# Optimization experiments

Measured on AMD Instinct MI355X. Metric: run time of the kernel, lower is better.

Reference implementation:

```python
import jax, jax.numpy as jnp
import numpy as np

NUM_HEADS = 8
EMBED_DIM = 128
HEAD_DIM = EMBED_DIM // NUM_HEADS  # 16
NB_FEATURES = EMBED_DIM            # 128
EPS = 1e-4


def _make_projection(nb_rows, nb_cols, rng):
    # gaussian_orthogonal_random_matrix with scaling=0
    blocks = []
    for _ in range(nb_rows // nb_cols):
        q, _ = np.linalg.qr(rng.standard_normal((nb_cols, nb_cols)))
        blocks.append(q.T)
    rem = nb_rows - (nb_rows // nb_cols) * nb_cols
    if rem > 0:
        q, _ = np.linalg.qr(rng.standard_normal((nb_cols, nb_cols)))
        blocks.append(q.T[:rem])
    final = np.concatenate(blocks, axis=0)
    mult = np.linalg.norm(rng.standard_normal((nb_rows, nb_cols)), axis=1)
    return (mult[:, None] * final).astype(np.float32)


def setup_inputs() -> dict:
    key = jax.random.key(0)
    ks = jax.random.split(key, 7)
    R, C, E = 8, 2048, EMBED_DIM
    s = 1.0 / np.sqrt(E)
    x = jax.random.normal(ks[0], (R, C, E), dtype=jnp.float32)
    Wq = jax.random.uniform(ks[1], (E, E), jnp.float32, -s, s)
    bq = jax.random.uniform(ks[2], (E,), jnp.float32, -s, s)
    Wk = jax.random.uniform(ks[3], (E, E), jnp.float32, -s, s)
    bk = jax.random.uniform(ks[4], (E,), jnp.float32, -s, s)
    Wv = jax.random.uniform(ks[5], (E, E), jnp.float32, -s, s)
    bv = jax.random.uniform(ks[6], (E,), jnp.float32, -s, s)
    proj = jnp.asarray(_make_projection(NB_FEATURES, HEAD_DIM, np.random.default_rng(0)))
    return {"x": x, "Wq": Wq, "bq": bq, "Wk": Wk, "bk": bk, "Wv": Wv, "bv": bv, "proj": proj}


def _softmax_kernel(data, proj, is_query):
    # data: (R, h, n, d); proj: (F, d)
    d = data.shape[-1]
    normalizer = d ** (-0.25)
    ratio = proj.shape[0] ** (-0.5)
    data_dash = jnp.einsum('rhnd,jd->rhnj', normalizer * data, proj)  # (R,h,n,F)
    diag = jnp.sum(data * data, axis=-1, keepdims=True) * 0.5 * normalizer ** 2
    if is_query:
        m = jnp.max(data_dash, axis=-1, keepdims=True)
    else:
        m = jnp.max(data_dash, axis=(-1, -2), keepdims=True)
    return ratio * (jnp.exp(data_dash - diag - m) + EPS)


def reference(x, Wq, bq, Wk, bk, Wv, bv, proj):
    R, C, E = x.shape
    h, hd = NUM_HEADS, HEAD_DIM

    def proj_heads(W, b):
        y = jnp.einsum('rce,fe->rcf', x, W) + b
        return y.reshape(R, C, h, hd).transpose(0, 2, 1, 3)  # (R,h,C,hd)

    q = _softmax_kernel(proj_heads(Wq, bq), proj, is_query=True)   # (R,h,C,F)
    k = _softmax_kernel(proj_heads(Wk, bk), proj, is_query=False)  # (R,h,C,F)
    v = proj_heads(Wv, bv)                                          # (R,h,C,hd)

    # fold batch (R) into the feature dim: (h, C, R*F) / (h, C, R*hd)
    qf = q.transpose(1, 2, 0, 3).reshape(h, C, R * NB_FEATURES)
    kf = k.transpose(1, 2, 0, 3).reshape(h, C, R * NB_FEATURES)
    vf = v.transpose(1, 2, 0, 3).reshape(h, C, R * hd)

    k_sum = kf.sum(axis=-2)                                   # (h, D)
    D_inv = 1.0 / jnp.einsum('hnd,hd->hn', qf, k_sum)         # (h, C)
    context = jnp.einsum('hnd,hne->hde', kf, vf)              # (h, D, Ev)
    out = jnp.einsum('hde,hnd,hn->hne', context, qf, D_inv)   # (h, C, R*hd)

    out = out.reshape(h, C, R, hd).transpose(2, 1, 0, 3).reshape(R, C, E)
    attn = jnp.einsum('hqf,hkf->hqk', qf, kf)                 # (h, C, C)
    return out, attn
```

## Files before the change

kernel.cpp:

```cpp
#include <hip/hip_runtime.h>
#include <hip/hip_bf16.h>
#include <stdint.h>

typedef __bf16 bf16x8 __attribute__((ext_vector_type(8)));
typedef float  f32x4  __attribute__((ext_vector_type(4)));

#define RATIO 0.08838834764831845f
#define EPSV  1e-4f

#define GLOBAL_AS __attribute__((address_space(1)))
#define LDS_AS    __attribute__((address_space(3)))

static __device__ __forceinline__ void gload16(const void* g, void* l) {
  __builtin_amdgcn_global_load_lds((GLOBAL_AS const void*)g, (LDS_AS void*)l, 16, 0, 0);
}

static constexpr size_t OFF_XB    = 0;
static constexpr size_t OFF_WCAT  = OFF_XB    + 4194304;
static constexpr size_t OFF_MQ    = OFF_WCAT  + 98304;
static constexpr size_t OFF_MK    = OFF_MQ    + 262144;
static constexpr size_t OFF_BCAT  = OFF_MK    + 262144;
static constexpr size_t OFF_BQF   = OFF_BCAT  + 2048;
static constexpr size_t OFF_BKF   = OFF_BQF   + 4096;
static constexpr size_t OFF_Y     = OFF_BKF   + 4096;
static constexpr size_t OFF_QF    = OFF_Y     + 25165824;
static constexpr size_t OFF_KF    = OFF_QF    + 33554432;
static constexpr size_t OFF_KFT   = OFF_KF    + 33554432;
static constexpr size_t OFF_VFT   = OFF_KFT   + 33554432;
static constexpr size_t OFF_KPART = OFF_VFT   + 4194304;
static constexpr size_t OFF_KMAX  = OFF_KPART + 4096;
static constexpr size_t OFF_KSUM  = OFF_KMAX  + 256;
static constexpr size_t OFF_DINV  = OFF_KSUM  + 32768;
static constexpr size_t OFF_CTXP  = OFF_DINV  + 65536;
static constexpr size_t OFF_CTXT  = OFF_CTXP  + 16777216;
static constexpr size_t WS_NEED   = OFF_CTXT  + 2097152;

static __device__ __forceinline__ void gemm_core(
    const __hip_bfloat16* __restrict__ A, const __hip_bfloat16* __restrict__ B,
    int lda, int ldb, int K, int tm, int tn,
    __bf16* As, __bf16* Bs, f32x4 acc[4][4]) {
  const int t    = threadIdx.x;
  const int w    = t >> 6;
  const int lane = t & 63;
  const int m_off = (w >> 1) << 6;
  const int n_off = (w & 1) << 6;
  const int r0 = t >> 2;
  const int kk = (t & 3) << 3;
  char* Asb = (char*)As + (w << 10);
  char* Bsb = (char*)Bs + (w << 10);
  const int frow = lane & 15;
  const int koff = (lane >> 4) << 3;
  for (int k0 = 0; k0 < K; k0 += 32) {
    const __hip_bfloat16* Ag = A + (size_t)(tm + r0) * lda + (k0 + kk);
    const __hip_bfloat16* Bg = B + (size_t)(tn + r0) * ldb + (k0 + kk);
    gload16(Ag, Asb);
    gload16(Ag + (size_t)64 * lda, Asb + 4096);
    gload16(Bg, Bsb);
    gload16(Bg + (size_t)64 * ldb, Bsb + 4096);
    __syncthreads();
    bf16x8 af[4], bfr[4];
#pragma unroll
    for (int mi = 0; mi < 4; ++mi)
      af[mi] = *(const bf16x8*)(As + ((m_off + mi * 16 + frow) << 5) + koff);
#pragma unroll
    for (int ni = 0; ni < 4; ++ni)
      bfr[ni] = *(const bf16x8*)(Bs + ((n_off + ni * 16 + frow) << 5) + koff);
#pragma unroll
    for (int mi = 0; mi < 4; ++mi)
#pragma unroll
      for (int ni = 0; ni < 4; ++ni)
        acc[mi][ni] = __builtin_amdgcn_mfma_f32_16x16x32_bf16(af[mi], bfr[ni], acc[mi][ni], 0, 0, 0);
    __syncthreads();
  }
}

#define ZERO_ACC(acc) do {                                   \
  _Pragma("unroll") for (int a_ = 0; a_ < 4; ++a_)           \
  _Pragma("unroll") for (int b_ = 0; b_ < 4; ++b_)           \
    acc[a_][b_] = (f32x4){0.f, 0.f, 0.f, 0.f};               \
} while (0)

__global__ void k_prep(const float* __restrict__ x,
                       const float* __restrict__ Wq, const float* __restrict__ bq,
                       const float* __restrict__ Wk, const float* __restrict__ bk,
                       const float* __restrict__ Wv, const float* __restrict__ bv,
                       const float* __restrict__ proj,
                       __hip_bfloat16* __restrict__ xb,
                       __hip_bfloat16* __restrict__ Wcat, float* __restrict__ bcat,
                       __hip_bfloat16* __restrict__ Mq, __hip_bfloat16* __restrict__ Mk,
                       float* __restrict__ bqf, float* __restrict__ bkf) {
  const int b = blockIdx.x, t = threadIdx.x;
  {
    int i = (b * 256 + t) * 4;
    f32x4 v = *(const f32x4*)(x + i);
#pragma unroll
    for (int j = 0; j < 4; ++j) xb[i + j] = __float2bfloat16(v[j]);
  }
  if (b < 1024) {
    int i = b * 256 + t;
    {
      int which = i >> 17;
      int rem = i & 131071;
      int hj = rem >> 7, e = rem & 127;
      int hh = hj >> 7, j = hj & 127;
      const float* W = which ? Wk : Wq;
      float s = 0.f;
#pragma unroll
      for (int u = 0; u < 16; ++u) s += proj[j * 16 + u] * W[(hh * 16 + u) * 128 + e];
      if (which) Mk[rem] = __float2bfloat16(0.5f * s);
      else       Mq[rem] = __float2bfloat16(0.5f * s);
    }
    if (i < 2048) {
      int which = i >> 10;
      int hj = i & 1023, hh = hj >> 7, j = hj & 127;
      const float* bb = which ? bk : bq;
      float s = 0.f;
#pragma unroll
      for (int u = 0; u < 16; ++u) s += proj[j * 16 + u] * bb[hh * 16 + u];
      if (which) bkf[hj] = 0.5f * s;
      else       bqf[hj] = 0.5f * s;
    }
  }
  if (b < 192) {
    int i = b * 256 + t;
    int mat = i >> 14, rem = i & 16383;
    const float* W = (mat == 0) ? Wq : ((mat == 1) ? Wk : Wv);
    Wcat[i] = __float2bfloat16(W[rem]);
    if (i < 384) {
      int m2 = i >> 7;
      const float* bb = (m2 == 0) ? bq : ((m2 == 1) ? bk : bv);
      bcat[i] = bb[i & 127];
    }
  }
}

__global__ __launch_bounds__(256) void k_proj(
    const __hip_bfloat16* __restrict__ xb, const __hip_bfloat16* __restrict__ Wcat,
    const float* __restrict__ bcat, float* __restrict__ Y) {
  __shared__ __align__(16) __bf16 As[4096], Bs[4096];
  const int tm = blockIdx.x << 7, tn = blockIdx.y << 7;
  f32x4 acc[4][4];
  ZERO_ACC(acc);
  gemm_core(xb, Wcat, 128, 128, 128, tm, tn, As, Bs, acc);
  const int t = threadIdx.x, w = t >> 6, lane = t & 63;
  const int m_off = (w >> 1) << 6, n_off = (w & 1) << 6;
#pragma unroll
  for (int ni = 0; ni < 4; ++ni) {
    const int col = tn + n_off + ni * 16 + (lane & 15);
    const float bias = bcat[col];
#pragma unroll
    for (int mi = 0; mi < 4; ++mi)
#pragma unroll
      for (int i = 0; i < 4; ++i) {
        const int row = tm + m_off + mi * 16 + ((lane >> 4) << 2) + i;
        Y[(size_t)row * 384 + col] = acc[mi][ni][i] + bias;
      }
  }
}

__global__ void k_vft2(const float* __restrict__ Y, __hip_bfloat16* __restrict__ vfT) {
  const int cb = blockIdx.x, r = blockIdx.y, h = blockIdx.z;
  const int c0 = cb << 7;
  __shared__ float tile[16][132];
  const int t = threadIdx.x;
  const int a = t & 15, cc0 = t >> 4;
#pragma unroll
  for (int i = 0; i < 8; ++i) {
    const int cc = cc0 + (i << 4);
    tile[a][cc] = Y[(size_t)(r * 2048 + c0 + cc) * 384 + 256 + (h << 4) + a];
  }
  __syncthreads();
  const int row = t >> 4, cg = t & 15;
  bf16x8 v;
#pragma unroll
  for (int j = 0; j < 8; ++j) v[j] = (__bf16)tile[row][(cg << 3) + j];
  *(bf16x8*)(vfT + ((size_t)((h << 7) + (r << 4) + row) << 11) + c0 + (cg << 3)) = v;
}

__global__ __launch_bounds__(256) void k_dashq(
    const __hip_bfloat16* __restrict__ xb, const __hip_bfloat16* __restrict__ Mq,
    const float* __restrict__ bqf, const float* __restrict__ Y,
    __hip_bfloat16* __restrict__ qf) {
  __shared__ __align__(16) __bf16 As[4096], Bs[4096];
  __shared__ float diag_s[128];
  __shared__ float rmax_s[2][128];
  const int h = blockIdx.y;
  const int tm = blockIdx.x << 7;
  f32x4 acc[4][4];
  ZERO_ACC(acc);
  gemm_core(xb, Mq + h * 16384, 128, 128, 128, tm, 0, As, Bs, acc);
  const int t = threadIdx.x, w = t >> 6, lane = t & 63;
  const int m_off = (w >> 1) << 6, n_off = (w & 1) << 6;
  if (t < 128) {
    const float* yp = Y + (size_t)(tm + t) * 384 + h * 16;
    float s = 0.f;
#pragma unroll
    for (int u = 0; u < 16; ++u) s += yp[u] * yp[u];
    diag_s[t] = 0.125f * s;
  }
  float bia[4];
#pragma unroll
  for (int ni = 0; ni < 4; ++ni) bia[ni] = bqf[h * 128 + n_off + ni * 16 + (lane & 15)];
  float rmx[4][4];
#pragma unroll
  for (int mi = 0; mi < 4; ++mi)
#pragma unroll
    for (int i = 0; i < 4; ++i) {
      float m0 = acc[mi][0][i] + bia[0];
      m0 = fmaxf(m0, acc[mi][1][i] + bia[1]);
      m0 = fmaxf(m0, acc[mi][2][i] + bia[2]);
      m0 = fmaxf(m0, acc[mi][3][i] + bia[3]);
      rmx[mi][i] = m0;
    }
#pragma unroll
  for (int off = 1; off < 16; off <<= 1)
#pragma unroll
    for (int mi = 0; mi < 4; ++mi)
#pragma unroll
      for (int i = 0; i < 4; ++i)
        rmx[mi][i] = fmaxf(rmx[mi][i], __shfl_xor(rmx[mi][i], off));
  if ((lane & 15) == 0) {
#pragma unroll
    for (int mi = 0; mi < 4; ++mi)
#pragma unroll
      for (int i = 0; i < 4; ++i)
        rmax_s[w & 1][m_off + mi * 16 + ((lane >> 4) << 2) + i] = rmx[mi][i];
  }
  __syncthreads();
#pragma unroll
  for (int mi = 0; mi < 4; ++mi) {
#pragma unroll
    for (int i = 0; i < 4; ++i) {
      const int rl = m_off + mi * 16 + ((lane >> 4) << 2) + i;
      const int rg = tm + rl;
      const int c = rg & 2047, r = rg >> 11;
      const float md = diag_s[rl] + fmaxf(rmax_s[0][rl], rmax_s[1][rl]);
#pragma unroll
      for (int ni = 0; ni < 4; ++ni) {
        const int j = n_off + ni * 16 + (lane & 15);
        const float f = RATIO * (__expf(acc[mi][ni][i] + bia[ni] - md) + EPSV);
        qf[((size_t)((h << 11) + c) << 10) + (r << 7) + j] = __float2bfloat16(f);
      }
    }
  }
}

__global__ __launch_bounds__(256) void k_dashk_max(
    const __hip_bfloat16* __restrict__ xb, const __hip_bfloat16* __restrict__ Mk,
    const float* __restrict__ bkf, float* __restrict__ kpart) {
  __shared__ __align__(16) __bf16 As[4096], Bs[4096];
  __shared__ float wmax[4];
  const int h = blockIdx.y;
  const int tm = blockIdx.x << 7;
  f32x4 acc[4][4];
  ZERO_ACC(acc);
  gemm_core(xb, Mk + h * 16384, 128, 128, 128, tm, 0, As, Bs, acc);
  const int t = threadIdx.x, w = t >> 6, lane = t & 63;
  const int n_off = (w & 1) << 6;
  float mx = -1e30f;
#pragma unroll
  for (int ni = 0; ni < 4; ++ni) {
    const float bia = bkf[h * 128 + n_off + ni * 16 + (lane & 15)];
#pragma unroll
    for (int mi = 0; mi < 4; ++mi)
#pragma unroll
      for (int i = 0; i < 4; ++i) mx = fmaxf(mx, acc[mi][ni][i] + bia);
  }
#pragma unroll
  for (int off = 1; off < 64; off <<= 1) mx = fmaxf(mx, __shfl_xor(mx, off));
  if (lane == 0) wmax[w] = mx;
  __syncthreads();
  if (t == 0) kpart[h * 128 + blockIdx.x] = fmaxf(fmaxf(wmax[0], wmax[1]), fmaxf(wmax[2], wmax[3]));
}

__global__ void k_kmaxred(const float* __restrict__ kpart, float* __restrict__ kmax) {
  const int t = threadIdx.x;
  const int r = t >> 3, h = t & 7;
  float m = -1e30f;
  for (int i = 0; i < 16; ++i) m = fmaxf(m, kpart[h * 128 + r * 16 + i]);
  kmax[r * 8 + h] = m;
}

__global__ __launch_bounds__(256) void k_dashk_feat(
    const __hip_bfloat16* __restrict__ xb, const __hip_bfloat16* __restrict__ Mk,
    const float* __restrict__ bkf, const float* __restrict__ Y,
    const float* __restrict__ kmax,
    __hip_bfloat16* __restrict__ kf, __hip_bfloat16* __restrict__ kfT) {
  __shared__ __align__(16) __bf16 As[4096], Bs[4096];
  __shared__ float diag_s[128];
  __shared__ __align__(16) __bf16 kT[128 * 136];
  const int h = blockIdx.y;
  const int tm = blockIdx.x << 7;
  f32x4 acc[4][4];
  ZERO_ACC(acc);
  gemm_core(xb, Mk + h * 16384, 128, 128, 128, tm, 0, As, Bs, acc);
  const int t = threadIdx.x, w = t >> 6, lane = t & 63;
  const int m_off = (w >> 1) << 6, n_off = (w & 1) << 6;
  if (t < 128) {
    const float* yp = Y + (size_t)(tm + t) * 384 + 128 + h * 16;
    float s = 0.f;
#pragma unroll
    for (int u = 0; u < 16; ++u) s += yp[u] * yp[u];
    diag_s[t] = 0.125f * s;
  }
  const int r = tm >> 11;
  const int c0 = tm & 2047;
  const float m = kmax[r * 8 + h];
  float bia[4];
#pragma unroll
  for (int ni = 0; ni < 4; ++ni) bia[ni] = bkf[h * 128 + n_off + ni * 16 + (lane & 15)];
  __syncthreads();
#pragma unroll
  for (int mi = 0; mi < 4; ++mi) {
#pragma unroll
    for (int i = 0; i < 4; ++i) {
      const int rl = m_off + mi * 16 + ((lane >> 4) << 2) + i;
      const int c = c0 + rl;
      const float dm = diag_s[rl] + m;
#pragma unroll
      for (int ni = 0; ni < 4; ++ni) {
        const int j = n_off + ni * 16 + (lane & 15);
        const float f = RATIO * (__expf(acc[mi][ni][i] + bia[ni] - dm) + EPSV);
        kf[((size_t)((h << 11) + c) << 10) + (r << 7) + j] = __float2bfloat16(f);
        kT[j * 136 + rl] = (__bf16)f;
      }
    }
  }
  __syncthreads();
  const int j2 = t >> 1, half = t & 1;
  __bf16* dst = (__bf16*)kfT + (((size_t)(h << 10) + (r << 7) + j2) << 11) + c0 + (half << 6);
  const __bf16* srcr = kT + j2 * 136 + (half << 6);
#pragma unroll
  for (int q8 = 0; q8 < 8; ++q8)
    *(bf16x8*)(dst + (q8 << 3)) = *(const bf16x8*)(srcr + (q8 << 3));
}

__global__ __launch_bounds__(256) void k_ksum2(const __hip_bfloat16* __restrict__ kfT,
                                               float* __restrict__ ksum) {
  const int t = threadIdx.x, w = t >> 6, lane = t & 63;
  const int row = blockIdx.x * 4 + w;
  const __bf16* p = (const __bf16*)kfT + ((size_t)row << 11);
  float s = 0.f;
#pragma unroll
  for (int q = 0; q < 4; ++q) {
    bf16x8 v = *(const bf16x8*)(p + ((lane + (q << 6)) << 3));
#pragma unroll
    for (int j = 0; j < 8; ++j) s += (float)v[j];
  }
#pragma unroll
  for (int off = 1; off < 64; off <<= 1) s += __shfl_xor(s, off);
  if (lane == 0) ksum[row] = s;
}

__global__ __launch_bounds__(256) void k_dinv(
    const __hip_bfloat16* __restrict__ qf, const float* __restrict__ ksum,
    float* __restrict__ dinv) {
  const int t = threadIdx.x, w = t >> 6, lane = t & 63;
  const int h = blockIdx.y;
  const int c = blockIdx.x * 4 + w;
  const __bf16* qp = (const __bf16*)qf + ((size_t)((h << 11) + c) << 10);
  const float* ks = ksum + h * 1024;
  const int d0 = lane << 4;
  bf16x8 v0 = *(const bf16x8*)(qp + d0);
  bf16x8 v1 = *(const bf16x8*)(qp + d0 + 8);
  float s = 0.f;
#pragma unroll
  for (int j = 0; j < 8; ++j) s += (float)v0[j] * ks[d0 + j] + (float)v1[j] * ks[d0 + 8 + j];
#pragma unroll
  for (int off = 1; off < 64; off <<= 1) s += __shfl_xor(s, off);
  if (lane == 0) dinv[(h << 11) + c] = 1.0f / s;
}

#define SBAR() __builtin_amdgcn_s_barrier()
#define FEN()  do { asm volatile("" ::: "memory"); __builtin_amdgcn_sched_barrier(0); } while (0)
#define PRIO1() __builtin_amdgcn_s_setprio(1)
#define PRIO0() __builtin_amdgcn_s_setprio(0)
#define VMW4() do { asm volatile("s_waitcnt vmcnt(4)" ::: "memory"); } while (0)
#define VMW0() do { asm volatile("s_waitcnt vmcnt(0)" ::: "memory"); } while (0)

#define MFMA16(nlo) do {                                                      \
  _Pragma("unroll") for (int mi_ = 0; mi_ < 8; ++mi_)                         \
  _Pragma("unroll") for (int nj_ = 0; nj_ < 2; ++nj_)                         \
    acc[mi_][(nlo) + nj_] = __builtin_amdgcn_mfma_f32_16x16x32_bf16(          \
        aR[mi_], bR[nj_], acc[mi_][(nlo) + nj_], 0, 0, 0);                    \
} while (0)

__global__ __launch_bounds__(512, 2) void k_attn8(
    const __hip_bfloat16* __restrict__ qf, const __hip_bfloat16* __restrict__ kf,
    float* __restrict__ attn) {
  extern __shared__ __align__(128) char lds[];
  const int lid = blockIdx.x;
  const int swz = ((lid & 7) << 6) + (lid >> 3);
  const int h  = swz >> 6;
  const int tm = ((swz >> 3) & 7) << 8;
  const int tn = (swz & 7) << 8;
  const __hip_bfloat16* Ag = qf + ((size_t)h << 21);
  const __hip_bfloat16* Bg = kf + ((size_t)h << 21);

  const int t = threadIdx.x, wid = t >> 6, lane = t & 63;
  const int f = lane & 15;
  const int wr = wid >> 2, wc = wid & 3;
  const int swzg = (((lane >> 4) ^ ((f >> 1) & 3)) << 4);
  const int aoff = ((wr << 7) + f) * 64 + swzg;
  const int boff = 65536 + ((wc << 6) + f) * 64 + swzg;
  const int srow = t >> 2;
  const int scol = (((t & 3) ^ ((t >> 3) & 3)) << 3);
  const int sdst = wid << 10;

  f32x4 acc[8][4] = {};
  bf16x8 aR[8], bR[2];

  auto stageA = [&](int buf, int kh, int k0) {
    char* d = lds + buf * 32768 + kh * 16384 + sdst;
    const __hip_bfloat16* g = Ag + (size_t)(tm + srow) * 1024 + k0 + (kh << 5) + scol;
    gload16(g, d);
    gload16(g + 128 * 1024, d + 8192);
  };
  auto stageB = [&](int buf, int kh, int k0) {
    char* d = lds + 65536 + buf * 32768 + kh * 16384 + sdst;
    const __hip_bfloat16* g = Bg + (size_t)(tn + srow) * 1024 + k0 + (kh << 5) + scol;
    gload16(g, d);
    gload16(g + 128 * 1024, d + 8192);
  };

  stageA(0, 0, 0); stageB(0, 0, 0); stageA(0, 1, 0); stageB(0, 1, 0);
  VMW4();
  SBAR(); FEN();

  for (int kt = 0; kt < 15; ++kt) {
    const int buf = kt & 1, nbuf = buf ^ 1;
    const int bo = buf * 32768;
    const int nk0 = (kt + 1) << 6;
#pragma unroll
    for (int mi = 0; mi < 8; ++mi) aR[mi] = *(const bf16x8*)(lds + bo + aoff + mi * 1024);
    bR[0] = *(const bf16x8*)(lds + bo + boff);
    bR[1] = *(const bf16x8*)(lds + bo + boff + 1024);
    stageA(nbuf, 0, nk0);
    PRIO1(); MFMA16(0); PRIO0();
    SBAR(); FEN();
    bR[0] = *(const bf16x8*)(lds + bo + boff + 2048);
    bR[1] = *(const bf16x8*)(lds + bo + boff + 3072);
    stageB(nbuf, 0, nk0);
    PRIO1(); MFMA16(2); PRIO0();
    VMW4();
    SBAR(); FEN();
#pragma unroll
    for (int mi = 0; mi < 8; ++mi) aR[mi] = *(const bf16x8*)(lds + bo + 16384 + aoff + mi * 1024);
    bR[0] = *(const bf16x8*)(lds + bo + 16384 + boff);
    bR[1] = *(const bf16x8*)(lds + bo + 16384 + boff + 1024);
    stageA(nbuf, 1, nk0);
    PRIO1(); MFMA16(0); PRIO0();
    SBAR(); FEN();
    bR[0] = *(const bf16x8*)(lds + bo + 16384 + boff + 2048);
    bR[1] = *(const bf16x8*)(lds + bo + 16384 + boff + 3072);
    stageB(nbuf, 1, nk0);
    PRIO1(); MFMA16(2); PRIO0();
    VMW4();
    SBAR(); FEN();
  }
  {
    const int bo = 32768;
#pragma unroll
    for (int mi = 0; mi < 8; ++mi) aR[mi] = *(const bf16x8*)(lds + bo + aoff + mi * 1024);
    bR[0] = *(const bf16x8*)(lds + bo + boff);
    bR[1] = *(const bf16x8*)(lds + bo + boff + 1024);
    PRIO1(); MFMA16(0); PRIO0();
    bR[0] = *(const bf16x8*)(lds + bo + boff + 2048);
    bR[1] = *(const bf16x8*)(lds + bo + boff + 3072);
    PRIO1(); MFMA16(2); PRIO0();
    VMW0();
    SBAR(); FEN();
#pragma unroll
    for (int mi = 0; mi < 8; ++mi) aR[mi] = *(const bf16x8*)(lds + bo + 16384 + aoff + mi * 1024);
    bR[0] = *(const bf16x8*)(lds + bo + 16384 + boff);
    bR[1] = *(const bf16x8*)(lds + bo + 16384 + boff + 1024);
    PRIO1(); MFMA16(0); PRIO0();
    bR[0] = *(const bf16x8*)(lds + bo + 16384 + boff + 2048);
    bR[1] = *(const bf16x8*)(lds + bo + 16384 + boff + 3072);
    PRIO1(); MFMA16(2); PRIO0();
  }

  float* Cc = attn + ((size_t)h << 22);
  const int rbase = tm + (wr << 7) + ((lane >> 4) << 2);
  const int cbase = tn + (wc << 6) + f;
#pragma unroll
  for (int mi = 0; mi < 8; ++mi)
#pragma unroll
    for (int i = 0; i < 4; ++i) {
      float* rp = Cc + ((size_t)(rbase + mi * 16 + i) << 11) + cbase;
#pragma unroll
      for (int ni = 0; ni < 4; ++ni) rp[ni * 16] = acc[mi][ni][i];
    }
}

__global__ __launch_bounds__(256) void k_ctx(
    const __hip_bfloat16* __restrict__ vfT, const __hip_bfloat16* __restrict__ kfT,
    float* __restrict__ ctxp) {
  __shared__ __align__(16) __bf16 As[4096], Bs[4096];
  const int z = blockIdx.z, h = z >> 2, kc = z & 3;
  const int tn = blockIdx.y << 7;
  f32x4 acc[4][4];
  ZERO_ACC(acc);
  gemm_core(vfT + ((size_t)h << 18) + (kc << 9), kfT + ((size_t)h << 21) + (kc << 9),
            2048, 2048, 512, 0, tn, As, Bs, acc);
  float* Cp = ctxp + ((size_t)(kc * 8 + h) << 17);
  const int t = threadIdx.x, w = t >> 6, lane = t & 63;
  const int m_off = (w >> 1) << 6, n_off = (w & 1) << 6;
#pragma unroll
  for (int mi = 0; mi < 4; ++mi)
#pragma unroll
    for (int i = 0; i < 4; ++i) {
      const int row = m_off + mi * 16 + ((lane >> 4) << 2) + i;
#pragma unroll
      for (int ni = 0; ni < 4; ++ni) {
        const int col = tn + n_off + ni * 16 + (lane & 15);
        Cp[((size_t)row << 10) + col] = acc[mi][ni][i];
      }
    }
}

__global__ void k_ctxred(const float* __restrict__ ctxp, __hip_bfloat16* __restrict__ ctxT) {
  const int i = blockIdx.x * 256 + threadIdx.x;
  const float s = ctxp[i] + ctxp[i + 1048576] + ctxp[i + 2097152] + ctxp[i + 3145728];
  ctxT[i] = __float2bfloat16(s);
}

__global__ __launch_bounds__(256) void k_out(
    const __hip_bfloat16* __restrict__ qf, const __hip_bfloat16* __restrict__ ctxT,
    const float* __restrict__ dinv, float* __restrict__ outp) {
  __shared__ __align__(16) __bf16 As[4096], Bs[4096];
  const int h = blockIdx.z;
  const int tm = blockIdx.x << 7;
  f32x4 acc[4][4];
  ZERO_ACC(acc);
  gemm_core(qf + ((size_t)h << 21), ctxT + ((size_t)h << 17), 1024, 1024, 1024, tm, 0, As, Bs, acc);
  const int t = threadIdx.x, w = t >> 6, lane = t & 63;
  const int m_off = (w >> 1) << 6, n_off = (w & 1) << 6;
#pragma unroll
  for (int mi = 0; mi < 4; ++mi)
#pragma unroll
    for (int i = 0; i < 4; ++i) {
      const int row = tm + m_off + mi * 16 + ((lane >> 4) << 2) + i;
      const float dv = dinv[(h << 11) + row];
#pragma unroll
      for (int ni = 0; ni < 4; ++ni) {
        const int col = n_off + ni * 16 + (lane & 15);
        const int rb = col >> 4, tt = col & 15;
        outp[(((size_t)(rb << 11) + row) << 7) + (h << 4) + tt] = acc[mi][ni][i] * dv;
      }
    }
}

extern "C" void kernel_launch(void* const* d_in, const int* in_sizes, int n_in,
                              void* d_out, int out_size, void* d_ws, size_t ws_size,
                              hipStream_t stream) {
  const float* x    = (const float*)d_in[0];
  const float* Wq   = (const float*)d_in[1];
  const float* bq   = (const float*)d_in[2];
  const float* Wk   = (const float*)d_in[3];
  const float* bk   = (const float*)d_in[4];
  const float* Wv   = (const float*)d_in[5];
  const float* bv   = (const float*)d_in[6];
  const float* proj = (const float*)d_in[7];
  if (ws_size < WS_NEED) return;

  char* ws = (char*)d_ws;
  __hip_bfloat16* xb   = (__hip_bfloat16*)(ws + OFF_XB);
  __hip_bfloat16* Wcat = (__hip_bfloat16*)(ws + OFF_WCAT);
  __hip_bfloat16* Mq   = (__hip_bfloat16*)(ws + OFF_MQ);
  __hip_bfloat16* Mk   = (__hip_bfloat16*)(ws + OFF_MK);
  float* bcat = (float*)(ws + OFF_BCAT);
  float* bqf  = (float*)(ws + OFF_BQF);
  float* bkf  = (float*)(ws + OFF_BKF);
  float* Y    = (float*)(ws + OFF_Y);
  __hip_bfloat16* qf  = (__hip_bfloat16*)(ws + OFF_QF);
  __hip_bfloat16* kf  = (__hip_bfloat16*)(ws + OFF_KF);
  __hip_bfloat16* kfT = (__hip_bfloat16*)(ws + OFF_KFT);
  __hip_bfloat16* vfT = (__hip_bfloat16*)(ws + OFF_VFT);
  float* kpart = (float*)(ws + OFF_KPART);
  float* kmax  = (float*)(ws + OFF_KMAX);
  float* ksum  = (float*)(ws + OFF_KSUM);
  float* dinv  = (float*)(ws + OFF_DINV);
  float* ctxp  = (float*)(ws + OFF_CTXP);
  __hip_bfloat16* ctxT = (__hip_bfloat16*)(ws + OFF_CTXT);

  float* outp = (float*)d_out;
  float* attn = (float*)d_out + 2097152;

  static int attr_done = 0;
  if (!attr_done) {
    (void)hipFuncSetAttribute((const void*)k_attn8,
                              hipFuncAttributeMaxDynamicSharedMemorySize, 131072);
    attr_done = 1;
  }

  k_prep<<<dim3(2048), dim3(256), 0, stream>>>(x, Wq, bq, Wk, bk, Wv, bv, proj,
                                               xb, Wcat, bcat, Mq, Mk, bqf, bkf);
  k_proj<<<dim3(128, 3), dim3(256), 0, stream>>>(xb, Wcat, bcat, Y);
  k_vft2<<<dim3(16, 8, 8), dim3(256), 0, stream>>>(Y, vfT);
  k_dashq<<<dim3(128, 8), dim3(256), 0, stream>>>(xb, Mq, bqf, Y, qf);
  k_dashk_max<<<dim3(128, 8), dim3(256), 0, stream>>>(xb, Mk, bkf, kpart);
  k_kmaxred<<<dim3(1), dim3(64), 0, stream>>>(kpart, kmax);
  k_dashk_feat<<<dim3(128, 8), dim3(256), 0, stream>>>(xb, Mk, bkf, Y, kmax, kf, kfT);
  k_ksum2<<<dim3(2048), dim3(256), 0, stream>>>(kfT, ksum);
  k_dinv<<<dim3(512, 8), dim3(256), 0, stream>>>(qf, ksum, dinv);
  k_attn8<<<dim3(512), dim3(512), 131072, stream>>>(qf, kf, attn);
  k_ctx<<<dim3(1, 8, 32), dim3(256), 0, stream>>>(vfT, kfT, ctxp);
  k_ctxred<<<dim3(4096), dim3(256), 0, stream>>>(ctxp, ctxT);
  k_out<<<dim3(16, 1, 8), dim3(256), 0, stream>>>(qf, ctxT, dinv, outp);
}
```

Baseline: 201.5 us.

## Fuse Q/K feature GEMMs, atomic key max, fold ksum and dinv into ctx/out

Merges the query and key feature GEMMs into one kernel that shares the x tile. The per-(r,h) key max is now taken with an atomicMax on an order-preserving unsigned key, and the key logits are stored as fp16. A separate elementwise kernel then applies exp and writes kf/kfT. This removes the second key GEMM and the max-reduction launch. The key column sums move into the ctx GEMM's B-fragment loads, and the D_inv dot product moves into the out GEMM's main loop, which drops the ksum and dinv kernels. In exchange it adds a 32MB fp16 intermediate write and read, with some precision risk from storing the logits in fp16.

```diff
diff --git a/kernel.cpp b/kernel.cpp
--- a/kernel.cpp
+++ b/kernel.cpp
@@ -3,6 +3,7 @@
 #include <stdint.h>
 
 typedef __bf16 bf16x8 __attribute__((ext_vector_type(8)));
+typedef _Float16 f16x8 __attribute__((ext_vector_type(8)));
 typedef float  f32x4  __attribute__((ext_vector_type(4)));
 
 #define RATIO 0.08838834764831845f
@@ -13,6 +14,15 @@
 
 static __device__ __forceinline__ void gload16(const void* g, void* l) {
   __builtin_amdgcn_global_load_lds((GLOBAL_AS const void*)g, (LDS_AS void*)l, 16, 0, 0);
+}
+
+static __device__ __forceinline__ unsigned fkey(float f) {
+  unsigned b = __float_as_uint(f);
+  return (b & 0x80000000u) ? ~b : (b | 0x80000000u);
+}
+static __device__ __forceinline__ float funkey(unsigned k) {
+  unsigned b = (k & 0x80000000u) ? (k & 0x7FFFFFFFu) : ~k;
+  return __uint_as_float(b);
 }
 
 static constexpr size_t OFF_XB    = 0;
@@ -27,11 +37,10 @@
 static constexpr size_t OFF_KF    = OFF_QF    + 33554432;
 static constexpr size_t OFF_KFT   = OFF_KF    + 33554432;
 static constexpr size_t OFF_VFT   = OFF_KFT   + 33554432;
-static constexpr size_t OFF_KPART = OFF_VFT   + 4194304;
-static constexpr size_t OFF_KMAX  = OFF_KPART + 4096;
-static constexpr size_t OFF_KSUM  = OFF_KMAX  + 256;
-static constexpr size_t OFF_DINV  = OFF_KSUM  + 32768;
-static constexpr size_t OFF_CTXP  = OFF_DINV  + 65536;
+static constexpr size_t OFF_KMAXI = OFF_VFT   + 4194304;
+static constexpr size_t OFF_KSUMP = OFF_KMAXI + 1024;
+static constexpr size_t OFF_EK    = OFF_KSUMP + 131072;
+static constexpr size_t OFF_CTXP  = OFF_EK    + 33554432;
 static constexpr size_t OFF_CTXT  = OFF_CTXP  + 16777216;
 static constexpr size_t WS_NEED   = OFF_CTXT  + 2097152;
 
@@ -88,7 +97,8 @@
                        __hip_bfloat16* __restrict__ xb,
                        __hip_bfloat16* __restrict__ Wcat, float* __restrict__ bcat,
                        __hip_bfloat16* __restrict__ Mq, __hip_bfloat16* __restrict__ Mk,
-                       float* __restrict__ bqf, float* __restrict__ bkf) {
+                       float* __restrict__ bqf, float* __restrict__ bkf,
+                       unsigned* __restrict__ kmaxI) {
   const int b = blockIdx.x, t = threadIdx.x;
   {
     int i = (b * 256 + t) * 4;
@@ -96,6 +106,7 @@
 #pragma unroll
     for (int j = 0; j < 4; ++j) xb[i + j] = __float2bfloat16(v[j]);
   }
+  if (b == 0 && t < 64) kmaxI[t] = 0u;
   if (b < 1024) {
     int i = b * 256 + t;
     {
@@ -177,39 +188,84 @@
   *(bf16x8*)(vfT + ((size_t)((h << 7) + (r << 4) + row) << 11) + c0 + (cg << 3)) = v;
 }
 
-__global__ __launch_bounds__(256) void k_dashq(
+__global__ __launch_bounds__(256) void k_dashqk(
     const __hip_bfloat16* __restrict__ xb, const __hip_bfloat16* __restrict__ Mq,
-    const float* __restrict__ bqf, const float* __restrict__ Y,
-    __hip_bfloat16* __restrict__ qf) {
-  __shared__ __align__(16) __bf16 As[4096], Bs[4096];
-  __shared__ float diag_s[128];
+    const __hip_bfloat16* __restrict__ Mk, const float* __restrict__ bqf,
+    const float* __restrict__ bkf, const float* __restrict__ Y,
+    __hip_bfloat16* __restrict__ qf, _Float16* __restrict__ ek,
+    unsigned* __restrict__ kmaxI) {
+  __shared__ __align__(16) __bf16 As[4096], Bqs[4096], Bks[4096];
+  __shared__ float diagq_s[128], diagk_s[128];
   __shared__ float rmax_s[2][128];
+  __shared__ float wmax_s[4];
   const int h = blockIdx.y;
   const int tm = blockIdx.x << 7;
-  f32x4 acc[4][4];
-  ZERO_ACC(acc);
-  gemm_core(xb, Mq + h * 16384, 128, 128, 128, tm, 0, As, Bs, acc);
   const int t = threadIdx.x, w = t >> 6, lane = t & 63;
   const int m_off = (w >> 1) << 6, n_off = (w & 1) << 6;
+  const int r0 = t >> 2, kk = (t & 3) << 3;
+  char* Asb = (char*)As + (w << 10);
+  char* Bqb = (char*)Bqs + (w << 10);
+  char* Bkb = (char*)Bks + (w << 10);
+  const int frow = lane & 15, koff = (lane >> 4) << 3;
+  const __hip_bfloat16* Bq_ = Mq + h * 16384;
+  const __hip_bfloat16* Bk_ = Mk + h * 16384;
   if (t < 128) {
     const float* yp = Y + (size_t)(tm + t) * 384 + h * 16;
     float s = 0.f;
 #pragma unroll
     for (int u = 0; u < 16; ++u) s += yp[u] * yp[u];
-    diag_s[t] = 0.125f * s;
-  }
-  float bia[4];
-#pragma unroll
-  for (int ni = 0; ni < 4; ++ni) bia[ni] = bqf[h * 128 + n_off + ni * 16 + (lane & 15)];
+    diagq_s[t] = 0.125f * s;
+  } else {
+    const int tt = t - 128;
+    const float* yp = Y + (size_t)(tm + tt) * 384 + 128 + h * 16;
+    float s = 0.f;
+#pragma unroll
+    for (int u = 0; u < 16; ++u) s += yp[u] * yp[u];
+    diagk_s[tt] = 0.125f * s;
+  }
+  f32x4 accq[4][4], acck[4][4];
+  ZERO_ACC(accq); ZERO_ACC(acck);
+  for (int k0 = 0; k0 < 128; k0 += 32) {
+    const __hip_bfloat16* Ag = xb + (size_t)(tm + r0) * 128 + (k0 + kk);
+    const __hip_bfloat16* Bg1 = Bq_ + (size_t)r0 * 128 + (k0 + kk);
+    const __hip_bfloat16* Bg2 = Bk_ + (size_t)r0 * 128 + (k0 + kk);
+    gload16(Ag, Asb);  gload16(Ag + 64 * 128, Asb + 4096);
+    gload16(Bg1, Bqb); gload16(Bg1 + 64 * 128, Bqb + 4096);
+    gload16(Bg2, Bkb); gload16(Bg2 + 64 * 128, Bkb + 4096);
+    __syncthreads();
+    bf16x8 af[4], bq1[4], bk1[4];
+#pragma unroll
+    for (int mi = 0; mi < 4; ++mi)
+      af[mi] = *(const bf16x8*)(As + ((m_off + mi * 16 + frow) << 5) + koff);
+#pragma unroll
+    for (int ni = 0; ni < 4; ++ni) {
+      bq1[ni] = *(const bf16x8*)(Bqs + ((n_off + ni * 16 + frow) << 5) + koff);
+      bk1[ni] = *(const bf16x8*)(Bks + ((n_off + ni * 16 + frow) << 5) + koff);
+    }
+#pragma unroll
+    for (int mi = 0; mi < 4; ++mi)
+#pragma unroll
+      for (int ni = 0; ni < 4; ++ni) {
+        accq[mi][ni] = __builtin_amdgcn_mfma_f32_16x16x32_bf16(af[mi], bq1[ni], accq[mi][ni], 0, 0, 0);
+        acck[mi][ni] = __builtin_amdgcn_mfma_f32_16x16x32_bf16(af[mi], bk1[ni], acck[mi][ni], 0, 0, 0);
+      }
+    __syncthreads();
+  }
+  float biaq[4], biak[4];
+#pragma unroll
+  for (int ni = 0; ni < 4; ++ni) {
+    biaq[ni] = bqf[h * 128 + n_off + ni * 16 + frow];
+    biak[ni] = bkf[h * 128 + n_off + ni * 16 + frow];
+  }
   float rmx[4][4];
 #pragma unroll
   for (int mi = 0; mi < 4; ++mi)
 #pragma unroll
     for (int i = 0; i < 4; ++i) {
-      float m0 = acc[mi][0][i] + bia[0];
-      m0 = fmaxf(m0, acc[mi][1][i] + bia[1]);
-      m0 = fmaxf(m0, acc[mi][2][i] + bia[2]);
-      m0 = fmaxf(m0, acc[mi][3][i] + bia[3]);
+      float m0 = accq[mi][0][i] + biaq[0];
+      m0 = fmaxf(m0, accq[mi][1][i] + biaq[1]);
+      m0 = fmaxf(m0, accq[mi][2][i] + biaq[2]);
+      m0 = fmaxf(m0, accq[mi][3][i] + biaq[3]);
       rmx[mi][i] = m0;
     }
 #pragma unroll
@@ -219,112 +275,72 @@
 #pragma unroll
       for (int i = 0; i < 4; ++i)
         rmx[mi][i] = fmaxf(rmx[mi][i], __shfl_xor(rmx[mi][i], off));
-  if ((lane & 15) == 0) {
+  if (frow == 0) {
 #pragma unroll
     for (int mi = 0; mi < 4; ++mi)
 #pragma unroll
       for (int i = 0; i < 4; ++i)
         rmax_s[w & 1][m_off + mi * 16 + ((lane >> 4) << 2) + i] = rmx[mi][i];
   }
+  float mxk = -1e30f;
+#pragma unroll
+  for (int ni = 0; ni < 4; ++ni)
+#pragma unroll
+    for (int mi = 0; mi < 4; ++mi)
+#pragma unroll
+      for (int i = 0; i < 4; ++i) mxk = fmaxf(mxk, acck[mi][ni][i] + biak[ni]);
+#pragma unroll
+  for (int off = 1; off < 64; off <<= 1) mxk = fmaxf(mxk, __shfl_xor(mxk, off));
+  if (lane == 0) wmax_s[w] = mxk;
   __syncthreads();
+  const int r = tm >> 11;
+  if (t == 0) {
+    float bm = fmaxf(fmaxf(wmax_s[0], wmax_s[1]), fmaxf(wmax_s[2], wmax_s[3]));
+    atomicMax(&kmaxI[r * 8 + h], fkey(bm));
+  }
 #pragma unroll
   for (int mi = 0; mi < 4; ++mi) {
 #pragma unroll
     for (int i = 0; i < 4; ++i) {
       const int rl = m_off + mi * 16 + ((lane >> 4) << 2) + i;
       const int rg = tm + rl;
-      const int c = rg & 2047, r = rg >> 11;
-      const float md = diag_s[rl] + fmaxf(rmax_s[0][rl], rmax_s[1][rl]);
+      const int c = rg & 2047;
+      const float mdq = diagq_s[rl] + fmaxf(rmax_s[0][rl], rmax_s[1][rl]);
+      const float dk = diagk_s[rl];
 #pragma unroll
       for (int ni = 0; ni < 4; ++ni) {
-        const int j = n_off + ni * 16 + (lane & 15);
-        const float f = RATIO * (__expf(acc[mi][ni][i] + bia[ni] - md) + EPSV);
-        qf[((size_t)((h << 11) + c) << 10) + (r << 7) + j] = __float2bfloat16(f);
+        const int j = n_off + ni * 16 + frow;
+        const float fq = RATIO * (__expf(accq[mi][ni][i] + biaq[ni] - mdq) + EPSV);
+        qf[((size_t)((h << 11) + c) << 10) + (r << 7) + j] = __float2bfloat16(fq);
+        ek[((size_t)h << 21) + ((size_t)rg << 7) + j] = (_Float16)(acck[mi][ni][i] + biak[ni] - dk);
       }
     }
   }
 }
 
-__global__ __launch_bounds__(256) void k_dashk_max(
-    const __hip_bfloat16* __restrict__ xb, const __hip_bfloat16* __restrict__ Mk,
-    const float* __restrict__ bkf, float* __restrict__ kpart) {
-  __shared__ __align__(16) __bf16 As[4096], Bs[4096];
-  __shared__ float wmax[4];
-  const int h = blockIdx.y;
-  const int tm = blockIdx.x << 7;
-  f32x4 acc[4][4];
-  ZERO_ACC(acc);
-  gemm_core(xb, Mk + h * 16384, 128, 128, 128, tm, 0, As, Bs, acc);
-  const int t = threadIdx.x, w = t >> 6, lane = t & 63;
-  const int n_off = (w & 1) << 6;
-  float mx = -1e30f;
-#pragma unroll
-  for (int ni = 0; ni < 4; ++ni) {
-    const float bia = bkf[h * 128 + n_off + ni * 16 + (lane & 15)];
-#pragma unroll
-    for (int mi = 0; mi < 4; ++mi)
-#pragma unroll
-      for (int i = 0; i < 4; ++i) mx = fmaxf(mx, acc[mi][ni][i] + bia);
-  }
-#pragma unroll
-  for (int off = 1; off < 64; off <<= 1) mx = fmaxf(mx, __shfl_xor(mx, off));
-  if (lane == 0) wmax[w] = mx;
-  __syncthreads();
-  if (t == 0) kpart[h * 128 + blockIdx.x] = fmaxf(fmaxf(wmax[0], wmax[1]), fmaxf(wmax[2], wmax[3]));
-}
-
-__global__ void k_kmaxred(const float* __restrict__ kpart, float* __restrict__ kmax) {
+__global__ __launch_bounds__(256) void k_kfeat(
+    const _Float16* __restrict__ ek, const unsigned* __restrict__ kmaxI,
+    __hip_bfloat16* __restrict__ kf, __hip_bfloat16* __restrict__ kfT) {
+  __shared__ __align__(16) __bf16 kT[128 * 136];
+  const int h = blockIdx.y, tm = blockIdx.x << 7;
+  const int r = tm >> 11, c0 = tm & 2047;
+  const float m = funkey(kmaxI[r * 8 + h]);
   const int t = threadIdx.x;
-  const int r = t >> 3, h = t & 7;
-  float m = -1e30f;
-  for (int i = 0; i < 16; ++i) m = fmaxf(m, kpart[h * 128 + r * 16 + i]);
-  kmax[r * 8 + h] = m;
-}
-
-__global__ __launch_bounds__(256) void k_dashk_feat(
-    const __hip_bfloat16* __restrict__ xb, const __hip_bfloat16* __restrict__ Mk,
-    const float* __restrict__ bkf, const float* __restrict__ Y,
-    const float* __restrict__ kmax,
-    __hip_bfloat16* __restrict__ kf, __hip_bfloat16* __restrict__ kfT) {
-  __shared__ __align__(16) __bf16 As[4096], Bs[4096];
-  __shared__ float diag_s[128];
-  __shared__ __align__(16) __bf16 kT[128 * 136];
-  const int h = blockIdx.y;
-  const int tm = blockIdx.x << 7;
-  f32x4 acc[4][4];
-  ZERO_ACC(acc);
-  gemm_core(xb, Mk + h * 16384, 128, 128, 128, tm, 0, As, Bs, acc);
-  const int t = threadIdx.x, w = t >> 6, lane = t & 63;
-  const int m_off = (w >> 1) << 6, n_off = (w & 1) << 6;
-  if (t < 128) {
-    const float* yp = Y + (size_t)(tm + t) * 384 + 128 + h * 16;
-    float s = 0.f;
-#pragma unroll
-    for (int u = 0; u < 16; ++u) s += yp[u] * yp[u];
-    diag_s[t] = 0.125f * s;
-  }
-  const int r = tm >> 11;
-  const int c0 = tm & 2047;
-  const float m = kmax[r * 8 + h];
-  float bia[4];
-#pragma unroll
-  for (int ni = 0; ni < 4; ++ni) bia[ni] = bkf[h * 128 + n_off + ni * 16 + (lane & 15)];
-  __syncthreads();
-#pragma unroll
-  for (int mi = 0; mi < 4; ++mi) {
-#pragma unroll
-    for (int i = 0; i < 4; ++i) {
-      const int rl = m_off + mi * 16 + ((lane >> 4) << 2) + i;
-      const int c = c0 + rl;
-      const float dm = diag_s[rl] + m;
-#pragma unroll
-      for (int ni = 0; ni < 4; ++ni) {
-        const int j = n_off + ni * 16 + (lane & 15);
-        const float f = RATIO * (__expf(acc[mi][ni][i] + bia[ni] - dm) + EPSV);
-        kf[((size_t)((h << 11) + c) << 10) + (r << 7) + j] = __float2bfloat16(f);
-        kT[j * 136 + rl] = (__bf16)f;
-      }
-    }
+  const int rl = t >> 1, jh = (t & 1) << 6;
+  const f16x8* ep = (const f16x8*)(ek + ((size_t)h << 21) + ((size_t)(tm + rl) << 7) + jh);
+  const int c = c0 + rl;
+  __bf16* kfp = (__bf16*)kf + (((size_t)((h << 11) + c)) << 10) + (r << 7) + jh;
+#pragma unroll
+  for (int q8 = 0; q8 < 8; ++q8) {
+    f16x8 ev = ep[q8];
+    bf16x8 fv;
+#pragma unroll
+    for (int j = 0; j < 8; ++j) {
+      const float f = RATIO * (__expf((float)ev[j] - m) + EPSV);
+      fv[j] = (__bf16)f;
+      kT[(jh + q8 * 8 + j) * 136 + rl] = fv[j];
+    }
+    *(bf16x8*)(kfp + q8 * 8) = fv;
   }
   __syncthreads();
   const int j2 = t >> 1, half = t & 1;
@@ -333,42 +349,6 @@
 #pragma unroll
   for (int q8 = 0; q8 < 8; ++q8)
     *(bf16x8*)(dst + (q8 << 3)) = *(const bf16x8*)(srcr + (q8 << 3));
-}
-
-__global__ __launch_bounds__(256) void k_ksum2(const __hip_bfloat16* __restrict__ kfT,
-                                               float* __restrict__ ksum) {
-  const int t = threadIdx.x, w = t >> 6, lane = t & 63;
-  const int row = blockIdx.x * 4 + w;
-  const __bf16* p = (const __bf16*)kfT + ((size_t)row << 11);
-  float s = 0.f;
-#pragma unroll
-  for (int q = 0; q < 4; ++q) {
-    bf16x8 v = *(const bf16x8*)(p + ((lane + (q << 6)) << 3));
-#pragma unroll
-    for (int j = 0; j < 8; ++j) s += (float)v[j];
-  }
-#pragma unroll
-  for (int off = 1; off < 64; off <<= 1) s += __shfl_xor(s, off);
-  if (lane == 0) ksum[row] = s;
-}
-
-__global__ __launch_bounds__(256) void k_dinv(
-    const __hip_bfloat16* __restrict__ qf, const float* __restrict__ ksum,
-    float* __restrict__ dinv) {
-  const int t = threadIdx.x, w = t >> 6, lane = t & 63;
-  const int h = blockIdx.y;
-  const int c = blockIdx.x * 4 + w;
-  const __bf16* qp = (const __bf16*)qf + ((size_t)((h << 11) + c) << 10);
-  const float* ks = ksum + h * 1024;
-  const int d0 = lane << 4;
-  bf16x8 v0 = *(const bf16x8*)(qp + d0);
-  bf16x8 v1 = *(const bf16x8*)(qp + d0 + 8);
-  float s = 0.f;
-#pragma unroll
-  for (int j = 0; j < 8; ++j) s += (float)v0[j] * ks[d0 + j] + (float)v1[j] * ks[d0 + 8 + j];
-#pragma unroll
-  for (int off = 1; off < 64; off <<= 1) s += __shfl_xor(s, off);
-  if (lane == 0) dinv[(h << 11) + c] = 1.0f / s;
 }
 
 #define SBAR() __builtin_amdgcn_s_barrier()
@@ -495,17 +475,57 @@
 
 __global__ __launch_bounds__(256) void k_ctx(
     const __hip_bfloat16* __restrict__ vfT, const __hip_bfloat16* __restrict__ kfT,
-    float* __restrict__ ctxp) {
+    float* __restrict__ ctxp, float* __restrict__ ksump) {
   __shared__ __align__(16) __bf16 As[4096], Bs[4096];
   const int z = blockIdx.z, h = z >> 2, kc = z & 3;
   const int tn = blockIdx.y << 7;
+  const int t = threadIdx.x, w = t >> 6, lane = t & 63;
+  const int m_off = (w >> 1) << 6, n_off = (w & 1) << 6;
+  const int r0 = t >> 2, kk = (t & 3) << 3;
+  char* Asb = (char*)As + (w << 10);
+  char* Bsb = (char*)Bs + (w << 10);
+  const int frow = lane & 15, koff = (lane >> 4) << 3;
+  const __hip_bfloat16* A = vfT + ((size_t)h << 18) + (kc << 9);
+  const __hip_bfloat16* B = kfT + ((size_t)h << 21) + (kc << 9);
   f32x4 acc[4][4];
   ZERO_ACC(acc);
-  gemm_core(vfT + ((size_t)h << 18) + (kc << 9), kfT + ((size_t)h << 21) + (kc << 9),
-            2048, 2048, 512, 0, tn, As, Bs, acc);
-  float* Cp = ctxp + ((size_t)(kc * 8 + h) << 17);
-  const int t = threadIdx.x, w = t >> 6, lane = t & 63;
-  const int m_off = (w >> 1) << 6, n_off = (w & 1) << 6;
+  float bsum[4] = {0.f, 0.f, 0.f, 0.f};
+  for (int k0 = 0; k0 < 512; k0 += 32) {
+    const __hip_bfloat16* Ag = A + (size_t)r0 * 2048 + (k0 + kk);
+    const __hip_bfloat16* Bg = B + (size_t)(tn + r0) * 2048 + (k0 + kk);
+    gload16(Ag, Asb);
+    gload16(Ag + (size_t)64 * 2048, Asb + 4096);
+    gload16(Bg, Bsb);
+    gload16(Bg + (size_t)64 * 2048, Bsb + 4096);
+    __syncthreads();
+    bf16x8 af[4], bfr[4];
+#pragma unroll
+    for (int mi = 0; mi < 4; ++mi)
+      af[mi] = *(const bf16x8*)(As + ((m_off + mi * 16 + frow) << 5) + koff);
+#pragma unroll
+    for (int ni = 0; ni < 4; ++ni) {
+      bfr[ni] = *(const bf16x8*)(Bs + ((n_off + ni * 16 + frow) << 5) + koff);
+#pragma unroll
+      for (int j = 0; j < 8; ++j) bsum[ni] += (float)bfr[ni][j];
+    }
+#pragma unroll
+    for (int mi = 0; mi < 4; ++mi)
+#pragma unroll
+      for (int ni = 0; ni < 4; ++ni)
+        acc[mi][ni] = __builtin_amdgcn_mfma_f32_16x16x32_bf16(af[mi], bfr[ni], acc[mi][ni], 0, 0, 0);
+    __syncthreads();
+  }
+#pragma unroll
+  for (int ni = 0; ni < 4; ++ni) {
+    bsum[ni] += __shfl_xor(bsum[ni], 16);
+    bsum[ni] += __shfl_xor(bsum[ni], 32);
+  }
+  if (w < 2 && (lane >> 4) == 0) {
+#pragma unroll
+    for (int ni = 0; ni < 4; ++ni)
+      ksump[(((kc << 3) + h) << 10) + tn + n_off + ni * 16 + frow] = bsum[ni];
+  }
+  float* Cp = ctxp + ((size_t)((kc << 3) + h) << 17);
 #pragma unroll
   for (int mi = 0; mi < 4; ++mi)
 #pragma unroll
@@ -513,7 +533,7 @@
       const int row = m_off + mi * 16 + ((lane >> 4) << 2) + i;
 #pragma unroll
       for (int ni = 0; ni < 4; ++ni) {
-        const int col = tn + n_off + ni * 16 + (lane & 15);
+        const int col = tn + n_off + ni * 16 + frow;
         Cp[((size_t)row << 10) + col] = acc[mi][ni][i];
       }
     }
@@ -527,24 +547,73 @@
 
 __global__ __launch_bounds__(256) void k_out(
     const __hip_bfloat16* __restrict__ qf, const __hip_bfloat16* __restrict__ ctxT,
-    const float* __restrict__ dinv, float* __restrict__ outp) {
+    const float* __restrict__ ksump, float* __restrict__ outp) {
   __shared__ __align__(16) __bf16 As[4096], Bs[4096];
+  __shared__ float ksum_s[1024];
+  __shared__ float dsum_s[2][128];
   const int h = blockIdx.z;
   const int tm = blockIdx.x << 7;
+  const int t = threadIdx.x, w = t >> 6, lane = t & 63;
+  const int m_off = (w >> 1) << 6, n_off = (w & 1) << 6;
+  const int r0 = t >> 2, kk = (t & 3) << 3;
+  char* Asb = (char*)As + (w << 10);
+  char* Bsb = (char*)Bs + (w << 10);
+  const int frow = lane & 15, koff = (lane >> 4) << 3;
+  const __hip_bfloat16* A = qf + ((size_t)h << 21);
+  const __hip_bfloat16* B = ctxT + ((size_t)h << 17);
+#pragma unroll
+  for (int it = 0; it < 4; ++it) {
+    const int d = t + it * 256;
+    ksum_s[d] = ksump[(h << 10) + d] + ksump[((8 + h) << 10) + d] +
+                ksump[((16 + h) << 10) + d] + ksump[((24 + h) << 10) + d];
+  }
   f32x4 acc[4][4];
   ZERO_ACC(acc);
-  gemm_core(qf + ((size_t)h << 21), ctxT + ((size_t)h << 17), 1024, 1024, 1024, tm, 0, As, Bs, acc);
-  const int t = threadIdx.x, w = t >> 6, lane = t & 63;
-  const int m_off = (w >> 1) << 6, n_off = (w & 1) << 6;
+  const int drow = t & 127, dh = t >> 7;
+  const int dsw = (drow >> 1) & 3;
+  float dot = 0.f;
+  for (int k0 = 0; k0 < 1024; k0 += 32) {
+    const __hip_bfloat16* Ag = A + (size_t)(tm + r0) * 1024 + (k0 + kk);
+    const __hip_bfloat16* Bg = B + (size_t)r0 * 1024 + (k0 + kk);
+    gload16(Ag, Asb);
+    gload16(Ag + (size_t)64 * 1024, Asb + 4096);
+    gload16(Bg, Bsb);
+    gload16(Bg + (size_t)64 * 1024, Bsb + 4096);
+    __syncthreads();
+    bf16x8 af[4], bfr[4];
+#pragma unroll
+    for (int mi = 0; mi < 4; ++mi)
+      af[mi] = *(const bf16x8*)(As + ((m_off + mi * 16 + frow) << 5) + koff);
+#pragma unroll
+    for (int ni = 0; ni < 4; ++ni)
+      bfr[ni] = *(const bf16x8*)(Bs + ((n_off + ni * 16 + frow) << 5) + koff);
+#pragma unroll
+    for (int u = 0; u < 2; ++u) {
+      const int g = ((dh << 1) + u) ^ dsw;
+      bf16x8 av = *(const bf16x8*)((char*)As + drow * 64 + g * 16);
+      const float* kp = &ksum_s[k0 + (g << 3)];
+#pragma unroll
+      for (int j = 0; j < 8; ++j) dot += (float)av[j] * kp[j];
+    }
+#pragma unroll
+    for (int mi = 0; mi < 4; ++mi)
+#pragma unroll
+      for (int ni = 0; ni < 4; ++ni)
+        acc[mi][ni] = __builtin_amdgcn_mfma_f32_16x16x32_bf16(af[mi], bfr[ni], acc[mi][ni], 0, 0, 0);
+    __syncthreads();
+  }
+  dsum_s[dh][drow] = dot;
+  __syncthreads();
 #pragma unroll
   for (int mi = 0; mi < 4; ++mi)
 #pragma unroll
     for (int i = 0; i < 4; ++i) {
-      const int row = tm + m_off + mi * 16 + ((lane >> 4) << 2) + i;
-      const float dv = dinv[(h << 11) + row];
+      const int rl = m_off + mi * 16 + ((lane >> 4) << 2) + i;
+      const int row = tm + rl;
+      const float dv = 1.0f / (dsum_s[0][rl] + dsum_s[1][rl]);
 #pragma unroll
       for (int ni = 0; ni < 4; ++ni) {
-        const int col = n_off + ni * 16 + (lane & 15);
+        const int col = n_off + ni * 16 + frow;
         const int rb = col >> 4, tt = col & 15;
         outp[(((size_t)(rb << 11) + row) << 7) + (h << 4) + tt] = acc[mi][ni][i] * dv;
       }
@@ -577,10 +646,9 @@
   __hip_bfloat16* kf  = (__hip_bfloat16*)(ws + OFF_KF);
   __hip_bfloat16* kfT = (__hip_bfloat16*)(ws + OFF_KFT);
   __hip_bfloat16* vfT = (__hip_bfloat16*)(ws + OFF_VFT);
-  float* kpart = (float*)(ws + OFF_KPART);
-  float* kmax  = (float*)(ws + OFF_KMAX);
-  float* ksum  = (float*)(ws + OFF_KSUM);
-  float* dinv  = (float*)(ws + OFF_DINV);
+  unsigned* kmaxI = (unsigned*)(ws + OFF_KMAXI);
+  float* ksump = (float*)(ws + OFF_KSUMP);
+  _Float16* ek = (_Float16*)(ws + OFF_EK);
   float* ctxp  = (float*)(ws + OFF_CTXP);
   __hip_bfloat16* ctxT = (__hip_bfloat16*)(ws + OFF_CTXT);
 
@@ -595,17 +663,13 @@
   }
 
   k_prep<<<dim3(2048), dim3(256), 0, stream>>>(x, Wq, bq, Wk, bk, Wv, bv, proj,
-                                               xb, Wcat, bcat, Mq, Mk, bqf, bkf);
+                                               xb, Wcat, bcat, Mq, Mk, bqf, bkf, kmaxI);
   k_proj<<<dim3(128, 3), dim3(256), 0, stream>>>(xb, Wcat, bcat, Y);
   k_vft2<<<dim3(16, 8, 8), dim3(256), 0, stream>>>(Y, vfT);
-  k_dashq<<<dim3(128, 8), dim3(256), 0, stream>>>(xb, Mq, bqf, Y, qf);
-  k_dashk_max<<<dim3(128, 8), dim3(256), 0, stream>>>(xb, Mk, bkf, kpart);
-  k_kmaxred<<<dim3(1), dim3(64), 0, stream>>>(kpart, kmax);
-  k_dashk_feat<<<dim3(128, 8), dim3(256), 0, stream>>>(xb, Mk, bkf, Y, kmax, kf, kfT);
-  k_ksum2<<<dim3(2048), dim3(256), 0, stream>>>(kfT, ksum);
-  k_dinv<<<dim3(512, 8), dim3(256), 0, stream>>>(qf, ksum, dinv);
+  k_dashqk<<<dim3(128, 8), dim3(256), 0, stream>>>(xb, Mq, Mk, bqf, bkf, Y, qf, ek, kmaxI);
+  k_kfeat<<<dim3(128, 8), dim3(256), 0, stream>>>(ek, kmaxI, kf, kfT);
   k_attn8<<<dim3(512), dim3(512), 131072, stream>>>(qf, kf, attn);
-  k_ctx<<<dim3(1, 8, 32), dim3(256), 0, stream>>>(vfT, kfT, ctxp);
+  k_ctx<<<dim3(1, 8, 32), dim3(256), 0, stream>>>(vfT, kfT, ctxp, ksump);
   k_ctxred<<<dim3(4096), dim3(256), 0, stream>>>(ctxp, ctxT);
-  k_out<<<dim3(16, 1, 8), dim3(256), 0, stream>>>(qf, ctxT, dinv, outp);
-}
+  k_out<<<dim3(16, 1, 8), dim3(256), 0, stream>>>(qf, ctxT, ksump, outp);
+}
```

New measurement: 228.6 us. 13.4% more time.
